# Kernel tuning notes

Measured on AMD Instinct MI355X. Metric: run time of the kernel, lower is better.

Reference implementation:

```python
import jax, jax.numpy as jnp
import numpy as np

NUM_CLASSES = 64      # num_classes (centroid_mode='mean': extra_clusters/prototypes unused)
TEMP = 0.1            # contrastive_temp
GLW = 0.5             # global_loss_weight
N, D, B, K = 65536, 512, 4, 16


def setup_inputs() -> dict:
    key = jax.random.key(0)
    k1, k2, k3, k4 = jax.random.split(key, 4)
    S1 = jax.random.normal(k1, (N, D), dtype=jnp.float32)
    S2 = jax.random.normal(k2, (N, D), dtype=jnp.float32)
    seg = jax.random.randint(k3, (N,), 0, NUM_CLASSES)
    # guarantee every class appears, so torch.unique(labels) == arange(NUM_CLASSES)
    seg = seg.at[:NUM_CLASSES].set(jnp.arange(NUM_CLASSES))
    sim = jax.random.uniform(k4, (B, N // B, K), dtype=jnp.float32)
    return {"S1": S1, "S2": S2, "segmentation_map": seg,
            "similarity_matrix": sim}


def reference(S1, S2, segmentation_map, similarity_matrix):
    labels = segmentation_map.reshape(-1)  # [N] int; all classes present
    # --- compute_centroid (mean mode) as one-pass segment reduce ---
    ones = jnp.ones((labels.shape[0],), dtype=S1.dtype)
    counts = jax.ops.segment_sum(ones, labels, num_segments=NUM_CLASSES)      # [C]
    sums = jax.ops.segment_sum(S1, labels, num_segments=NUM_CLASSES)          # [C,D]
    centroids = sums / counts[:, None]                                        # [C,D]
    # --- logits ---
    local_logits = (S1 @ centroids.T) / TEMP    # [N,C]
    global_logits = (S2 @ centroids.T) / TEMP   # [N,C]
    # labels after mask/argmax remap equal the original labels (unique==arange)
    w = similarity_matrix.mean(axis=2).reshape(-1)  # [N]
    def ce(logits):
        logp = jax.nn.log_softmax(logits, axis=-1)
        return -jnp.take_along_axis(logp, labels[:, None], axis=1)[:, 0]
    local_loss = (ce(local_logits) * w).mean()
    global_loss = (ce(global_logits) * w).mean()
    return ((1.0 - GLW) * local_loss + GLW * global_loss) / 2.0
```

## Files before the change

kernel.cpp:

```cpp
#include <hip/hip_runtime.h>

#define NROWS 65536
#define DDIM  512
#define NCLS  64

typedef __attribute__((ext_vector_type(4))) float  floatx4;
typedef __attribute__((ext_vector_type(8))) short  shortx8;

static constexpr float SCALE = 0.25f / (float)NROWS;

static constexpr size_t OFF_SUMS   = 0;
static constexpr size_t OFF_HIST   = 131072;
static constexpr size_t OFF_CURSOR = 131328;
static constexpr size_t OFF_IDX    = 131584;

__device__ __forceinline__ unsigned short f2bf(float f) {
  unsigned u = __float_as_uint(f);
  return (unsigned short)((u + 0x7fffu + ((u >> 16) & 1u)) >> 16);
}

__global__ __launch_bounds__(256) void k_hist(const int* __restrict__ seg,
                                              int* __restrict__ hist) {
  __shared__ int h[NCLS];
  const int t = threadIdx.x;
  if (t < NCLS) h[t] = 0;
  __syncthreads();
  const int4 v = ((const int4*)seg)[blockIdx.x * 256 + t];
  atomicAdd(&h[v.x], 1); atomicAdd(&h[v.y], 1);
  atomicAdd(&h[v.z], 1); atomicAdd(&h[v.w], 1);
  __syncthreads();
  if (t < NCLS) atomicAdd(&hist[t], h[t]);
}

__global__ __launch_bounds__(1024) void k_scatter2(const int* __restrict__ seg,
                                                   const int* __restrict__ hist,
                                                   int* __restrict__ cursor,
                                                   int* __restrict__ idx) {
  __shared__ int lhist[NCLS];
  __shared__ int gbase[NCLS];
  const int t = threadIdx.x;
  if (t < NCLS) lhist[t] = 0;
  __syncthreads();
  const int i0 = blockIdx.x * 2048 + t;
  const int lab0 = seg[i0];
  const int r0 = atomicAdd(&lhist[lab0], 1);
  const int i1 = i0 + 1024;
  const int lab1 = seg[i1];
  const int r1 = atomicAdd(&lhist[lab1], 1);
  __syncthreads();
  if (t < NCLS) {
    const int h = hist[t];
    int x = h;
#pragma unroll
    for (int off = 1; off < 64; off <<= 1) {
      const int y = __shfl_up(x, off, 64);
      if (t >= off) x += y;
    }
    gbase[t] = (x - h) + atomicAdd(&cursor[t], lhist[t]);
  }
  __syncthreads();
  idx[gbase[lab0] + r0] = i0;
  idx[gbase[lab1] + r1] = i1;
}

__global__ __launch_bounds__(256) void k_sumsC(const float* __restrict__ S1,
                                               const int* __restrict__ idx,
                                               const int* __restrict__ hist,
                                               float* __restrict__ sums) {
  __shared__ int sh_start[NCLS + 1];
  __shared__ float red[256];
  const int c  = blockIdx.x >> 3;
  const int qq = blockIdx.x & 7;
  const int t  = threadIdx.x;
  if (t < 64) {
    const int h = hist[t];
    int x = h;
#pragma unroll
    for (int off = 1; off < 64; off <<= 1) {
      const int y = __shfl_up(x, off, 64);
      if (t >= off) x += y;
    }
    sh_start[t] = x - h;
    if (t == 63) sh_start[64] = x;
  }
  __syncthreads();
  const int s0 = sh_start[c];
  const int n  = sh_start[c + 1] - s0;
  const int sub = t >> 6;
  const int col = qq * 64 + (t & 63);
  const int n4 = n >> 2;
  const int base = s0 + sub * n4;
  const int len  = (sub == 3) ? (n - 3 * n4) : n4;
  const float* Sc = S1 + col;
  const int* ip = idx + base;
  float a0 = 0.f, a1 = 0.f, a2 = 0.f, a3 = 0.f;
  int j = 0;
  if (len >= 8) {
    int r[8];
#pragma unroll
    for (int q = 0; q < 8; ++q) r[q] = ip[q];
    for (; j + 16 <= len; j += 8) {
      int nr[8];
#pragma unroll
      for (int q = 0; q < 8; ++q) nr[q] = ip[j + 8 + q];
      a0 += Sc[(size_t)r[0] * DDIM]; a1 += Sc[(size_t)r[1] * DDIM];
      a2 += Sc[(size_t)r[2] * DDIM]; a3 += Sc[(size_t)r[3] * DDIM];
      a0 += Sc[(size_t)r[4] * DDIM]; a1 += Sc[(size_t)r[5] * DDIM];
      a2 += Sc[(size_t)r[6] * DDIM]; a3 += Sc[(size_t)r[7] * DDIM];
#pragma unroll
      for (int q = 0; q < 8; ++q) r[q] = nr[q];
    }
    a0 += Sc[(size_t)r[0] * DDIM]; a1 += Sc[(size_t)r[1] * DDIM];
    a2 += Sc[(size_t)r[2] * DDIM]; a3 += Sc[(size_t)r[3] * DDIM];
    a0 += Sc[(size_t)r[4] * DDIM]; a1 += Sc[(size_t)r[5] * DDIM];
    a2 += Sc[(size_t)r[6] * DDIM]; a3 += Sc[(size_t)r[7] * DDIM];
    j += 8;
  }
  for (; j < len; ++j) a0 += Sc[(size_t)idx[base + j] * DDIM];
  red[t] = a0 + a1 + a2 + a3;
  __syncthreads();
  if (t < 64)
    sums[(size_t)c * DDIM + col] = red[t] + red[t + 64] + red[t + 128] + red[t + 192];
}

__global__ __launch_bounds__(512, 4) void k_loss(const float* __restrict__ S1,
                                                 const float* __restrict__ S2,
                                                 const int* __restrict__ seg,
                                                 const float* __restrict__ sim,
                                                 const float* __restrict__ sums,
                                                 const int* __restrict__ hist,
                                                 float* __restrict__ out) {
  __shared__ short cent[NCLS * DDIM];
  __shared__ float red8[8];
  const int t = threadIdx.x;

  {
    const int cls = t >> 3;
    const float inv = 10.0f / (float)hist[cls];
    const float* sp = sums + (size_t)cls * DDIM;
#pragma unroll
    for (int i = 0; i < 8; ++i) {
      const int g = (t & 7) + i * 8;
      const float4 x = *(const float4*)(sp + g * 8);
      const float4 y = *(const float4*)(sp + g * 8 + 4);
      shortx8 b;
      b[0] = (short)f2bf(x.x * inv); b[1] = (short)f2bf(x.y * inv);
      b[2] = (short)f2bf(x.z * inv); b[3] = (short)f2bf(x.w * inv);
      b[4] = (short)f2bf(y.x * inv); b[5] = (short)f2bf(y.y * inv);
      b[6] = (short)f2bf(y.z * inv); b[7] = (short)f2bf(y.w * inv);
      *(shortx8*)&cent[cls * DDIM + ((g ^ (cls & 7)) * 8)] = b;
    }
  }
  __syncthreads();

  const int w    = t >> 6;
  const int lane = t & 63;
  const int n    = lane & 15;
  const int quad = lane >> 4;
  const int vb   = blockIdx.x * 256;
  const bool isS2 = (vb >= NROWS);
  const float* S = isS2 ? S2 : S1;
  const int i0m = isS2 ? (vb - NROWS) : vb;

  float loss_acc = 0.f;
#pragma unroll 1
  for (int s = 0; s < 2; ++s) {
    const int row0 = i0m + s * 128 + w * 16;
    const float* Srow = S + (size_t)(row0 + n) * DDIM;
    floatx4 acc0 = {0,0,0,0}, acc1 = {0,0,0,0}, acc2 = {0,0,0,0}, acc3 = {0,0,0,0};
    float4 aLo = *(const float4*)(Srow + quad * 8);
    float4 aHi = *(const float4*)(Srow + quad * 8 + 4);
#pragma unroll 1
    for (int c = 0; c < 16; ++c) {
      const int cn = (c + 1) & 15;
      const float4 nLo = *(const float4*)(Srow + cn * 32 + quad * 8);
      const float4 nHi = *(const float4*)(Srow + cn * 32 + quad * 8 + 4);
      shortx8 af;
      af[0] = (short)f2bf(aLo.x); af[1] = (short)f2bf(aLo.y);
      af[2] = (short)f2bf(aLo.z); af[3] = (short)f2bf(aLo.w);
      af[4] = (short)f2bf(aHi.x); af[5] = (short)f2bf(aHi.y);
      af[6] = (short)f2bf(aHi.z); af[7] = (short)f2bf(aHi.w);
      const int gp = ((c * 4 + quad) ^ (n & 7)) * 8;
      const shortx8 b0 = *(const shortx8*)&cent[(0  + n) * DDIM + gp];
      acc0 = __builtin_amdgcn_mfma_f32_16x16x32_bf16(af, b0, acc0, 0, 0, 0);
      const shortx8 b1 = *(const shortx8*)&cent[(16 + n) * DDIM + gp];
      acc1 = __builtin_amdgcn_mfma_f32_16x16x32_bf16(af, b1, acc1, 0, 0, 0);
      const shortx8 b2 = *(const shortx8*)&cent[(32 + n) * DDIM + gp];
      acc2 = __builtin_amdgcn_mfma_f32_16x16x32_bf16(af, b2, acc2, 0, 0, 0);
      const shortx8 b3 = *(const shortx8*)&cent[(48 + n) * DDIM + gp];
      acc3 = __builtin_amdgcn_mfma_f32_16x16x32_bf16(af, b3, acc3, 0, 0, 0);
      aLo = nLo; aHi = nHi;
    }
#pragma unroll
    for (int r = 0; r < 4; ++r) {
      float mx = fmaxf(fmaxf(acc0[r], acc1[r]), fmaxf(acc2[r], acc3[r]));
      mx = fmaxf(mx, __shfl_xor(mx, 1, 16));
      mx = fmaxf(mx, __shfl_xor(mx, 2, 16));
      mx = fmaxf(mx, __shfl_xor(mx, 4, 16));
      mx = fmaxf(mx, __shfl_xor(mx, 8, 16));
      float se = __expf(acc0[r] - mx) + __expf(acc1[r] - mx) +
                 __expf(acc2[r] - mx) + __expf(acc3[r] - mx);
      se += __shfl_xor(se, 1, 16);
      se += __shfl_xor(se, 2, 16);
      se += __shfl_xor(se, 4, 16);
      se += __shfl_xor(se, 8, 16);
      const int lab = seg[row0 + quad * 4 + r];
      const int ctl = lab >> 4, nl = lab & 15;
      float v = (ctl == 0) ? acc0[r] : (ctl == 1) ? acc1[r]
              : (ctl == 2) ? acc2[r] : acc3[r];
      const float lv = __shfl(v, nl, 16);
      const float ce = mx + __logf(se) - lv;
      if (n == r) {
        const int R = row0 + quad * 4 + r;
        const float4* sp4 = (const float4*)&sim[(size_t)R * 16];
        const float4 w0 = sp4[0], w1 = sp4[1], w2 = sp4[2], w3 = sp4[3];
        const float wgt = (w0.x + w0.y + w0.z + w0.w + w1.x + w1.y + w1.z + w1.w +
                           w2.x + w2.y + w2.z + w2.w + w3.x + w3.y + w3.z + w3.w) * (1.0f / 16.0f);
        loss_acc += ce * wgt;
      }
    }
  }

  float v = loss_acc * SCALE;
#pragma unroll
  for (int off = 1; off < 64; off <<= 1) v += __shfl_xor(v, off, 64);
  if (lane == 0) red8[w] = v;
  __syncthreads();
  if (t == 0) {
    float sacc = red8[0] + red8[1] + red8[2] + red8[3] +
                 red8[4] + red8[5] + red8[6] + red8[7];
    atomicAdd(out, sacc);
  }
}

extern "C" void kernel_launch(void* const* d_in, const int* in_sizes, int n_in,
                              void* d_out, int out_size, void* d_ws, size_t ws_size,
                              hipStream_t stream) {
  const float* S1  = (const float*)d_in[0];
  const float* S2  = (const float*)d_in[1];
  const int*   seg = (const int*)d_in[2];
  const float* sim = (const float*)d_in[3];
  char* ws = (char*)d_ws;
  float* sums   = (float*)(ws + OFF_SUMS);
  int*   hist   = (int*)(ws + OFF_HIST);
  int*   cursor = (int*)(ws + OFF_CURSOR);
  int*   idx    = (int*)(ws + OFF_IDX);
  float* out = (float*)d_out;

  hipMemsetAsync(ws + OFF_HIST, 0, 512, stream);
  hipMemsetAsync(d_out, 0, sizeof(float), stream);

  k_hist<<<64, 256, 0, stream>>>(seg, hist);
  k_scatter2<<<32, 1024, 0, stream>>>(seg, hist, cursor, idx);
  k_sumsC<<<512, 256, 0, stream>>>(S1, idx, hist, sums);
  k_loss<<<512, 512, 0, stream>>>(S1, S2, seg, sim, sums, hist, out);
}
```

Measured before the change: 310.7 us.

## Split class rows across blocks with full-row float4 gathers and atomic sums

```diff
diff --git a/kernel.cpp b/kernel.cpp
--- a/kernel.cpp
+++ b/kernel.cpp
@@ -35,10 +35,12 @@
 __global__ __launch_bounds__(1024) void k_scatter2(const int* __restrict__ seg,
                                                    const int* __restrict__ hist,
                                                    int* __restrict__ cursor,
-                                                   int* __restrict__ idx) {
+                                                   int* __restrict__ idx,
+                                                   float* __restrict__ sums) {
   __shared__ int lhist[NCLS];
   __shared__ int gbase[NCLS];
   const int t = threadIdx.x;
+  sums[blockIdx.x * 1024 + t] = 0.f;
   if (t < NCLS) lhist[t] = 0;
   __syncthreads();
   const int i0 = blockIdx.x * 2048 + t;
@@ -68,10 +70,10 @@
                                                const int* __restrict__ hist,
                                                float* __restrict__ sums) {
   __shared__ int sh_start[NCLS + 1];
-  __shared__ float red[256];
-  const int c  = blockIdx.x >> 3;
-  const int qq = blockIdx.x & 7;
-  const int t  = threadIdx.x;
+  __shared__ floatx4 red4[128];
+  const int c = blockIdx.x >> 3;
+  const int g = blockIdx.x & 7;
+  const int t = threadIdx.x;
   if (t < 64) {
     const int h = hist[t];
     int x = h;
@@ -86,41 +88,43 @@
   __syncthreads();
   const int s0 = sh_start[c];
   const int n  = sh_start[c + 1] - s0;
-  const int sub = t >> 6;
-  const int col = qq * 64 + (t & 63);
-  const int n4 = n >> 2;
-  const int base = s0 + sub * n4;
-  const int len  = (sub == 3) ? (n - 3 * n4) : n4;
-  const float* Sc = S1 + col;
+  const int seg8 = n >> 3;
+  const int base = s0 + g * seg8;
+  const int len  = (g == 7) ? (n - 7 * seg8) : seg8;
+
+  const int col4 = (t & 127) * 4;
+  const int slot = t >> 7;
   const int* ip = idx + base;
-  float a0 = 0.f, a1 = 0.f, a2 = 0.f, a3 = 0.f;
-  int j = 0;
+  floatx4 acc = {0.f, 0.f, 0.f, 0.f};
+  int j = slot;
   if (len >= 8) {
-    int r[8];
-#pragma unroll
-    for (int q = 0; q < 8; ++q) r[q] = ip[q];
-    for (; j + 16 <= len; j += 8) {
-      int nr[8];
-#pragma unroll
-      for (int q = 0; q < 8; ++q) nr[q] = ip[j + 8 + q];
-      a0 += Sc[(size_t)r[0] * DDIM]; a1 += Sc[(size_t)r[1] * DDIM];
-      a2 += Sc[(size_t)r[2] * DDIM]; a3 += Sc[(size_t)r[3] * DDIM];
-      a0 += Sc[(size_t)r[4] * DDIM]; a1 += Sc[(size_t)r[5] * DDIM];
-      a2 += Sc[(size_t)r[6] * DDIM]; a3 += Sc[(size_t)r[7] * DDIM];
-#pragma unroll
-      for (int q = 0; q < 8; ++q) r[q] = nr[q];
-    }
-    a0 += Sc[(size_t)r[0] * DDIM]; a1 += Sc[(size_t)r[1] * DDIM];
-    a2 += Sc[(size_t)r[2] * DDIM]; a3 += Sc[(size_t)r[3] * DDIM];
-    a0 += Sc[(size_t)r[4] * DDIM]; a1 += Sc[(size_t)r[5] * DDIM];
-    a2 += Sc[(size_t)r[6] * DDIM]; a3 += Sc[(size_t)r[7] * DDIM];
-    j += 8;
-  }
-  for (; j < len; ++j) a0 += Sc[(size_t)idx[base + j] * DDIM];
-  red[t] = a0 + a1 + a2 + a3;
-  __syncthreads();
-  if (t < 64)
-    sums[(size_t)c * DDIM + col] = red[t] + red[t + 64] + red[t + 128] + red[t + 192];
+    int ra = ip[j], rb = ip[j + 2];
+    for (; j + 6 < len; j += 4) {
+      const int na = ip[j + 4];
+      const int nb = ip[j + 6];
+      const floatx4 va = *(const floatx4*)(S1 + (size_t)ra * DDIM + col4);
+      const floatx4 vb = *(const floatx4*)(S1 + (size_t)rb * DDIM + col4);
+      acc = acc + va + vb;
+      ra = na; rb = nb;
+    }
+    acc = acc + *(const floatx4*)(S1 + (size_t)ra * DDIM + col4);
+    if (j + 2 < len)
+      acc = acc + *(const floatx4*)(S1 + (size_t)rb * DDIM + col4);
+    j += 4;
+  }
+  for (; j < len; j += 2)
+    acc = acc + *(const floatx4*)(S1 + (size_t)ip[j] * DDIM + col4);
+
+  if (slot == 1) red4[t & 127] = acc;
+  __syncthreads();
+  if (slot == 0) {
+    const floatx4 s = acc + red4[t];
+    float* dst = &sums[(size_t)c * DDIM + col4];
+    atomicAdd(dst + 0, s[0]);
+    atomicAdd(dst + 1, s[1]);
+    atomicAdd(dst + 2, s[2]);
+    atomicAdd(dst + 3, s[3]);
+  }
 }
 
 __global__ __launch_bounds__(512, 4) void k_loss(const float* __restrict__ S1,
@@ -251,7 +255,7 @@
   hipMemsetAsync(d_out, 0, sizeof(float), stream);
 
   k_hist<<<64, 256, 0, stream>>>(seg, hist);
-  k_scatter2<<<32, 1024, 0, stream>>>(seg, hist, cursor, idx);
+  k_scatter2<<<32, 1024, 0, stream>>>(seg, hist, cursor, idx, sums);
   k_sumsC<<<512, 256, 0, stream>>>(S1, idx, hist, sums);
   k_loss<<<512, 512, 0, stream>>>(S1, S2, seg, sim, sums, hist, out);
 }
```

Result: no change. 309.3 us (-0.4%).
